# Kernel optimization log

Hardware: AMD Instinct MI355X
Metric: run time of the kernel (lower is better)

Reference implementation:

```python
import jax, jax.numpy as jnp
import numpy as np

IM = 256          # image size (square)
GRID = 512        # oversampled NUFFT grid
J = 6             # Kaiser-Bessel kernel width (torchkbnufft default numpoints)
ALPHA = GRID / IM
BETA = float(np.pi * np.sqrt((J / ALPHA) ** 2 * (ALPHA - 0.5) ** 2 - 0.8))  # Fessler 'best' beta
SC0 = float(np.sinh(BETA) / BETA)
B, C = 1, 8
N_SPOKES, N_SAMPLES = 256, 512
K = N_SPOKES * N_SAMPLES


def _scale_2d():
    # deapodization (inverse FT of KB kernel), separable, normalized to 1 at center
    n = (jnp.arange(IM) - IM / 2) / GRID
    t = BETA ** 2 - (np.pi * J * n) ** 2
    sp = jnp.sqrt(jnp.maximum(t, 1e-12))
    sn = jnp.sqrt(jnp.maximum(-t, 1e-12))
    ft = jnp.where(t > 0, jnp.sinh(sp) / sp, jnp.sinc(sn / np.pi))
    sc = (SC0 / ft).astype(jnp.float32)
    return sc[:, None] * sc[None, :]  # (IM, IM)


def _interp_coords(ktraj):
    # ktraj (2, K) in [-pi, pi] -> J neighbor grid indices + KB weights per dim
    tm = ktraj * (GRID / (2.0 * np.pi))
    base = jnp.floor(tm - J / 2.0)
    j = jnp.arange(1, J + 1, dtype=tm.dtype)
    idx = base[:, :, None] + j                     # (2, K, J)
    u = tm[:, :, None] - idx                       # kernel-centered distance
    q = jnp.maximum(1.0 - (2.0 * u / J) ** 2, 0.0)
    w = jnp.i0(BETA * jnp.sqrt(q)) / J             # (2, K, J) KB weights
    gi = jnp.mod(idx, GRID).astype(jnp.int32)
    return gi[0], gi[1], w[0], w[1]                # iy, ix, wy, wx


def _nufft_fwd(img, coords, sc2):
    # img (B, C, IM, IM) complex -> (B, C, K) non-uniform k-space, 'ortho' norm
    iy, ix, wy, wx = coords
    pad = jnp.zeros(img.shape[:2] + (GRID, GRID), img.dtype)
    pad = pad.at[..., :IM, :IM].set(img * sc2)
    kg = jnp.fft.fft2(pad) / GRID                  # /sqrt(GRID*GRID)
    vals = kg[..., iy[:, :, None], ix[:, None, :]]           # (B,C,K,J,J)
    w2 = (wy[:, :, None] * wx[:, None, :]).astype(kg.dtype)  # (K,J,J)
    return jnp.sum(vals * w2, axis=(-2, -1))


def _nufft_adj(kdata, coords, sc2, smaps):
    # kdata (B, C, K) -> coil-combined image (B, 1, IM, IM), 'ortho' norm
    iy, ix, wy, wx = coords
    w2 = (wy[:, :, None] * wx[:, None, :]).astype(kdata.dtype)
    vals = (kdata[..., None, None] * w2).reshape(kdata.shape[:2] + (-1,))
    flat = (iy[:, :, None] * GRID + ix[:, None, :]).reshape(-1)
    grid = jnp.zeros(kdata.shape[:2] + (GRID * GRID,), kdata.dtype)
    grid = grid.at[:, :, flat].add(vals).reshape(kdata.shape[:2] + (GRID, GRID))
    img = jnp.fft.ifft2(grid) * GRID               # adjoint of fft2/GRID
    img = img[..., :IM, :IM] * sc2
    return jnp.sum(jnp.conj(smaps) * img, axis=1, keepdims=True)


def setup_inputs() -> dict:
    key = jax.random.key(0)
    ks = jax.random.split(key, 6)
    # golden-angle radial trajectory (2, K) in [-pi, pi]
    ga = np.pi * (3.0 - np.sqrt(5.0))
    ang = np.arange(N_SPOKES) * ga
    r = np.linspace(-np.pi, np.pi, N_SAMPLES, endpoint=False)
    ky = np.outer(np.sin(ang), r).reshape(-1)
    kx = np.outer(np.cos(ang), r).reshape(-1)
    ktraj = jnp.asarray(np.stack([ky, kx]), dtype=jnp.float32)
    return {
        "x": jax.random.normal(ks[0], (B, 1, IM, IM), jnp.float32),
        "y_real": jax.random.normal(ks[1], (B, C, K), jnp.float32),
        "y_imag": jax.random.normal(ks[2], (B, C, K), jnp.float32),
        "smaps_real": jax.random.normal(ks[3], (B, C, IM, IM), jnp.float32),
        "smaps_imag": jax.random.normal(ks[4], (B, C, IM, IM), jnp.float32),
        "ktraj": ktraj,
        "lambda_raw": jnp.full((1,), float(np.log(np.exp(1.0) - 1.0)), jnp.float32),
    }


def reference(x, y_real, y_imag, smaps_real, smaps_imag, ktraj, lambda_raw):
    sc2 = _scale_2d()
    coords = _interp_coords(ktraj)
    smaps = (smaps_real + 1j * smaps_imag).astype(jnp.complex64)
    y = (y_real + 1j * y_imag).astype(jnp.complex64)
    x_c = x.astype(jnp.complex64)
    coil_images = x_c * smaps                      # (B, C, IM, IM)
    A_x = _nufft_fwd(coil_images, coords, sc2)     # (B, C, K)
    lam = jax.nn.sigmoid(lambda_raw)[0].astype(jnp.complex64)
    k_dc = lam * A_x + (1.0 - lam) * y             # data consistency mix
    return _nufft_adj(k_dc, coords, sc2, smaps)    # (B, 1, IM, IM) complex64
```

## Files before the change

### kernel.cpp

```cpp
#include <hip/hip_runtime.h>
#include <math.h>

#define GRID_N 512
#define IM_N   256
#define NCOIL  8
#define NK     131072
#define PLANE  (GRID_N*GRID_N)
#define JW     6
#define NBIN   (GRID_N*GRID_N/512*512)
#define WSZ    11
#define NWIN   47
#define ACCROWS 528
#define BETA_F 13.8551003f
#define KSCALE 81.48733086305042f

struct cplx { float x, y; };

__device__ __forceinline__ float bessel_i0f(float x){
  if (x < 3.75f){
    float t = x*(1.0f/3.75f); t = t*t;
    return 1.0f + t*(3.5156229f + t*(3.0899424f + t*(1.2067492f
           + t*(0.2659732f + t*(0.0360768f + t*0.0045813f)))));
  } else {
    float t = 3.75f/x;
    float p = 0.39894228f + t*(0.01328592f + t*(0.00225319f + t*(-0.00157565f
            + t*(0.00916281f + t*(-0.02057706f + t*(0.02635537f
            + t*(-0.01647633f + t*0.00392377f)))))));
    return p * __expf(x) * rsqrtf(x);
  }
}

__device__ __forceinline__ float kb_w(float u){
  float uu = u*(1.0f/3.0f);
  float q = fmaxf(1.0f - uu*uu, 0.0f);
  return bessel_i0f(BETA_F*sqrtf(q)) * (1.0f/6.0f);
}

__device__ __forceinline__ unsigned bf16_of(float f){
  unsigned u = __float_as_uint(f);
  return (u + 0x8000u) >> 16;
}
__device__ __forceinline__ float bf_lo(unsigned w){ return __uint_as_float(w << 16); }
__device__ __forceinline__ float bf_hi(unsigned w){ return __uint_as_float(w & 0xFFFF0000u); }

__global__ void k_sc_table(float* sc){
  int i = threadIdx.x;
  if (i >= IM_N) return;
  float n  = (i - IM_N*0.5f) * (1.0f/GRID_N);
  float pj = 3.14159265358979f * (float)JW * n;
  float t  = BETA_F*BETA_F - pj*pj;
  float sp = sqrtf(fmaxf(t, 1e-12f));
  float sn = sqrtf(fmaxf(-t, 1e-12f));
  float ft = (t > 0.0f) ? (sinhf(sp)/sp) : (sinf(sn)/sn);
  float sc0 = sinhf(BETA_F)/BETA_F;
  sc[i] = sc0/ft;
}

__global__ void k_zero1(float* p, int n){
  int i = blockIdx.x*blockDim.x + threadIdx.x;
  if (i < n) p[i] = 0.f;
}

__global__ void k_fft_fill(const float* __restrict__ ximg, const float* __restrict__ sr,
                           const float* __restrict__ si, const float* __restrict__ sc,
                           cplx* __restrict__ buf){
  __shared__ cplx lds[GRID_N];
  int blk = blockIdx.x;
  int c = blk >> 9, y = blk & (GRID_N-1);
  cplx* p = buf + (size_t)blk * GRID_N;
  int tid = threadIdx.x;
  if (y >= IM_N){
    cplx z; z.x = 0.f; z.y = 0.f;
    for (int i = tid; i < GRID_N; i += 256) p[i] = z;
    return;
  }
  float scy = sc[y];
  for (int i = tid; i < GRID_N; i += 256){
    int r = __brev((unsigned)i) >> 23;
    cplx v; v.x = 0.f; v.y = 0.f;
    if (i < IM_N){
      float vv = ximg[(y<<8)|i] * scy * sc[i];
      int gi = (c << 16) | (y << 8) | i;
      v.x = vv * sr[gi]; v.y = vv * si[gi];
    }
    lds[r] = v;
  }
  __syncthreads();
  for (int half = 1; half < GRID_N; half <<= 1){
    int j = tid & (half-1);
    int k = ((tid & ~(half-1)) << 1) | j;
    float ang = -3.14159265358979f * (float)j / (float)half;
    float sw, cw; __sincosf(ang, &sw, &cw);
    cplx u = lds[k];
    cplx v = lds[k+half];
    cplx t; t.x = v.x*cw - v.y*sw; t.y = v.x*sw + v.y*cw;
    lds[k].x      = u.x + t.x; lds[k].y      = u.y + t.y;
    lds[k+half].x = u.x - t.x; lds[k+half].y = u.y - t.y;
    __syncthreads();
  }
  for (int i = tid; i < GRID_N; i += 256) p[i] = lds[i];
}

template<int DIR>
__global__ void k_fft_rows(cplx* __restrict__ buf, float scale){
  __shared__ cplx lds[GRID_N];
  cplx* p = buf + (size_t)blockIdx.x * GRID_N;
  int tid = threadIdx.x;
  for (int i = tid; i < GRID_N; i += 256){
    int r = __brev((unsigned)i) >> 23;
    lds[r] = p[i];
  }
  __syncthreads();
  for (int half = 1; half < GRID_N; half <<= 1){
    int j = tid & (half-1);
    int k = ((tid & ~(half-1)) << 1) | j;
    float ang = (float)DIR * 3.14159265358979f * (float)j / (float)half;
    float sw, cw; __sincosf(ang, &sw, &cw);
    cplx u = lds[k];
    cplx v = lds[k+half];
    cplx t; t.x = v.x*cw - v.y*sw; t.y = v.x*sw + v.y*cw;
    lds[k].x      = u.x + t.x; lds[k].y      = u.y + t.y;
    lds[k+half].x = u.x - t.x; lds[k+half].y = u.y - t.y;
    __syncthreads();
  }
  for (int i = tid; i < GRID_N; i += 256){
    cplx v = lds[i]; v.x *= scale; v.y *= scale; p[i] = v;
  }
}

__global__ void k_transpose(const cplx* __restrict__ in, cplx* __restrict__ out){
  __shared__ cplx tile[32][33];
  int c  = blockIdx.z;
  int x0 = blockIdx.x*32, y0 = blockIdx.y*32;
  const cplx* ip = in  + (size_t)c*PLANE;
  cplx*       op = out + (size_t)c*PLANE;
  int tx = threadIdx.x, ty = threadIdx.y;
  for (int dy = 0; dy < 32; dy += 8)
    tile[ty+dy][tx] = ip[(size_t)(y0+ty+dy)*GRID_N + (x0+tx)];
  __syncthreads();
  for (int dy = 0; dy < 32; dy += 8)
    op[(size_t)(x0+ty+dy)*GRID_N + (y0+tx)] = tile[tx][ty+dy];
}

__global__ void k_c2i(const float2* __restrict__ plan, float2* __restrict__ inter){
  int t = blockIdx.x*blockDim.x + threadIdx.x;
  if (t >= PLANE*NCOIL) return;
  int c = t & 7; int cell = t >> 3;
  inter[(size_t)cell*8 + c] = plan[(size_t)c*PLANE + cell];
}

__global__ __launch_bounds__(256) void k_fwd(
    const float* __restrict__ ktraj, const float* __restrict__ yre,
    const float* __restrict__ yim, const float* __restrict__ lraw,
    const float4* __restrict__ KTi4, float4* __restrict__ kdc4){
  int t = blockIdx.x*blockDim.x + threadIdx.x;
  if (t >= NK*4) return;
  int k = t >> 2, p = t & 3;

  int iy[JW], ix[JW]; float wy[JW], wx[JW];
  {
    float tm = ktraj[k] * KSCALE;
    int base = (int)floorf(tm - 3.0f);
    #pragma unroll
    for (int j = 1; j <= JW; ++j){
      int fidx = base + j;
      wy[j-1] = kb_w(tm - (float)fidx);
      iy[j-1] = fidx & (GRID_N-1);
    }
  }
  {
    float tm = ktraj[NK + k] * KSCALE;
    int base = (int)floorf(tm - 3.0f);
    #pragma unroll
    for (int j = 1; j <= JW; ++j){
      int fidx = base + j;
      wx[j-1] = kb_w(tm - (float)fidx);
      ix[j-1] = fidx & (GRID_N-1);
    }
  }

  float ax=0.f, ay=0.f, az=0.f, aw=0.f;
  #pragma unroll
  for (int jx = 0; jx < JW; ++jx){
    int ox = ix[jx]*GRID_N;
    #pragma unroll
    for (int jy = 0; jy < JW; ++jy){
      float w2 = wx[jx]*wy[jy];
      float4 v = KTi4[(size_t)(ox + iy[jy])*4 + p];
      ax += w2*v.x; ay += w2*v.y; az += w2*v.z; aw += w2*v.w;
    }
  }
  float lam = 1.0f/(1.0f + __expf(-lraw[0]));
  float oml = 1.0f - lam;
  int c0 = 2*p;
  float4 o;
  o.x = lam*ax + oml*yre[(size_t)c0*NK + k];
  o.y = lam*ay + oml*yim[(size_t)c0*NK + k];
  o.z = lam*az + oml*yre[(size_t)(c0+1)*NK + k];
  o.w = lam*aw + oml*yim[(size_t)(c0+1)*NK + k];
  kdc4[(size_t)k*4 + p] = o;
}

__global__ void k_hist2(const float* __restrict__ ktraj, unsigned* __restrict__ hist2){
  int k = blockIdx.x*blockDim.x + threadIdx.x;
  if (k >= NK) return;
  float tmy = ktraj[k] * KSCALE;
  int by = ((int)floorf(tmy - 3.0f)) & (GRID_N-1);
  float tmx = ktraj[NK + k] * KSCALE;
  int bx = (int)floorf(tmx - 3.0f);
  #pragma unroll
  for (int j = 1; j <= JW; ++j){
    int cj = (bx + j) & (GRID_N-1);
    atomicAdd(&hist2[cj*GRID_N + by], 1u);
  }
}

__global__ void k_colscan(const unsigned* __restrict__ hist2,
                          unsigned* __restrict__ binOff,
                          unsigned* __restrict__ colTotal){
  __shared__ unsigned s[GRID_N];
  int col = blockIdx.x, t = threadIdx.x;
  unsigned mine = hist2[col*GRID_N + t];
  s[t] = mine;
  __syncthreads();
  for (int off = 1; off < GRID_N; off <<= 1){
    unsigned add = (t >= off) ? s[t - off] : 0u;
    __syncthreads();
    s[t] += add;
    __syncthreads();
  }
  binOff[col*GRID_N + t] = s[t] - mine;
  if (t == GRID_N-1) colTotal[col] = s[t];
}

__global__ void k_scanCT(const unsigned* __restrict__ colTotal,
                         unsigned* __restrict__ colBase){
  __shared__ unsigned s[GRID_N];
  int t = threadIdx.x;
  unsigned mine = colTotal[t];
  s[t] = mine;
  __syncthreads();
  for (int off = 1; off < GRID_N; off <<= 1){
    unsigned add = (t >= off) ? s[t - off] : 0u;
    __syncthreads();
    s[t] += add;
    __syncthreads();
  }
  colBase[t] = s[t] - mine;
  if (t == GRID_N-1) colBase[GRID_N] = s[t];
}

__global__ void k_addbase(unsigned* __restrict__ binOff,
                          const unsigned* __restrict__ colBase){
  int i = blockIdx.x*blockDim.x + threadIdx.x;
  if (i > NBIN) return;
  if (i == NBIN){ binOff[i] = colBase[GRID_N]; return; }
  binOff[i] += colBase[i >> 9];
}

__global__ void k_place(const float* __restrict__ ktraj,
                        const unsigned* __restrict__ binOff,
                        unsigned* __restrict__ cnt2,
                        uint4* __restrict__ recs){
  int k = blockIdx.x*blockDim.x + threadIdx.x;
  if (k >= NK) return;
  float tmy = ktraj[k] * KSCALE;
  int by0 = (int)floorf(tmy - 3.0f);
  int by = by0 & (GRID_N-1);
  float wy[JW];
  #pragma unroll
  for (int j = 1; j <= JW; ++j) wy[j-1] = kb_w(tmy - (float)(by0 + j));

  float tmx = ktraj[NK + k] * KSCALE;
  int bx = (int)floorf(tmx - 3.0f);
  unsigned tag = ((unsigned)k << 9) | (unsigned)by;
  #pragma unroll
  for (int j = 1; j <= JW; ++j){
    int cj = (bx + j) & (GRID_N-1);
    float wx = kb_w(tmx - (float)(bx + j));
    uint4 rec;
    rec.x = bf16_of(wx*wy[0]) | (bf16_of(wx*wy[1]) << 16);
    rec.y = bf16_of(wx*wy[2]) | (bf16_of(wx*wy[3]) << 16);
    rec.z = bf16_of(wx*wy[4]) | (bf16_of(wx*wy[5]) << 16);
    rec.w = tag;
    int bin = cj*GRID_N + by;
    unsigned pos = binOff[bin] + atomicAdd(&cnt2[bin], 1u);
    recs[pos] = rec;
  }
}

__global__ __launch_bounds__(512) void k_adj(
    const uint4* __restrict__ recs, const unsigned* __restrict__ binOff,
    const float* __restrict__ kdcf, cplx* __restrict__ Hp){
  __shared__ float accs[ACCROWS*8];
  __shared__ float part[2][8][16][8];
  const int col = blockIdx.x, h = blockIdx.y;
  const int tid = threadIdx.x;
  const int wave = tid >> 6, lane = tid & 63;
  const int slot = lane >> 3, q = lane & 7;
  for (int i = tid; i < ACCROWS*8; i += 512) accs[i] = 0.f;
  __syncthreads();

  const unsigned* bo = binOff + (size_t)col*GRID_N;
  const size_t qoff = (size_t)(h*8 + q);
  int pb = 0;

  for (int wi = 0; wi < NWIN; ++wi){
    int b0 = wi*WSZ;
    int b1 = b0 + WSZ; if (b1 > GRID_N) b1 = GRID_N;
    unsigned s = bo[b0];
    unsigned e = bo[b1];
    if (s == e) continue;

    float a0=0.f,a1=0.f,a2=0.f,a3=0.f,a4=0.f,a5=0.f,a6=0.f,a7=0.f;
    float a8=0.f,a9=0.f,a10=0.f,a11=0.f,a12=0.f,a13=0.f,a14=0.f,a15=0.f;

    for (unsigned base = s + (unsigned)wave*8; base < e; base += 64){
      unsigned e0 = base + (unsigned)slot;
      uint4 rc = recs[e0];
      float vv = 0.f;
      if (e0 < e){
        unsigned kk = (rc.w >> 9) & (NK-1);
        vv = kdcf[(size_t)kk*16 + qoff];
      }
      float w1 = bf_lo(rc.x), w2 = bf_hi(rc.x);
      float w3 = bf_lo(rc.y), w4 = bf_hi(rc.y);
      float w5 = bf_lo(rc.z), w6 = bf_hi(rc.z);
      int off = (int)(rc.w & (GRID_N-1)) - b0;
      #pragma unroll
      for (int r = 0; r < 16; ++r){
        int idx = r - off;
        float wlo = (idx < 2) ? w1 : ((idx < 4) ? w3 : w5);
        float whi = (idx < 2) ? w2 : ((idx < 4) ? w4 : w6);
        float w = (idx & 1) ? whi : wlo;
        w = ((unsigned)idx < 6u) ? w : 0.f;
        float contrib = w * vv;
        if (r==0) a0+=contrib; else if (r==1) a1+=contrib;
        else if (r==2) a2+=contrib; else if (r==3) a3+=contrib;
        else if (r==4) a4+=contrib; else if (r==5) a5+=contrib;
        else if (r==6) a6+=contrib; else if (r==7) a7+=contrib;
        else if (r==8) a8+=contrib; else if (r==9) a9+=contrib;
        else if (r==10) a10+=contrib; else if (r==11) a11+=contrib;
        else if (r==12) a12+=contrib; else if (r==13) a13+=contrib;
        else if (r==14) a14+=contrib; else a15+=contrib;
      }
    }

    #pragma unroll
    for (int m = 8; m <= 32; m <<= 1){
      a0 += __shfl_xor(a0, m);  a1 += __shfl_xor(a1, m);
      a2 += __shfl_xor(a2, m);  a3 += __shfl_xor(a3, m);
      a4 += __shfl_xor(a4, m);  a5 += __shfl_xor(a5, m);
      a6 += __shfl_xor(a6, m);  a7 += __shfl_xor(a7, m);
      a8 += __shfl_xor(a8, m);  a9 += __shfl_xor(a9, m);
      a10 += __shfl_xor(a10, m); a11 += __shfl_xor(a11, m);
      a12 += __shfl_xor(a12, m); a13 += __shfl_xor(a13, m);
      a14 += __shfl_xor(a14, m); a15 += __shfl_xor(a15, m);
    }
    if (slot == 0){
      part[pb][wave][0][q]  = a0;  part[pb][wave][1][q]  = a1;
      part[pb][wave][2][q]  = a2;  part[pb][wave][3][q]  = a3;
      part[pb][wave][4][q]  = a4;  part[pb][wave][5][q]  = a5;
      part[pb][wave][6][q]  = a6;  part[pb][wave][7][q]  = a7;
      part[pb][wave][8][q]  = a8;  part[pb][wave][9][q]  = a9;
      part[pb][wave][10][q] = a10; part[pb][wave][11][q] = a11;
      part[pb][wave][12][q] = a12; part[pb][wave][13][q] = a13;
      part[pb][wave][14][q] = a14; part[pb][wave][15][q] = a15;
    }
    __syncthreads();
    if (tid < 128){
      int r = tid >> 3, qq = tid & 7;
      float sum = part[pb][0][r][qq] + part[pb][1][r][qq]
                + part[pb][2][r][qq] + part[pb][3][r][qq]
                + part[pb][4][r][qq] + part[pb][5][r][qq]
                + part[pb][6][r][qq] + part[pb][7][r][qq];
      accs[(size_t)(b0+1+r)*8 + qq] += sum;
    }
    pb ^= 1;
  }
  __syncthreads();

  for (int i = tid; i < GRID_N*4; i += 512){
    int j = i >> 9, y = i & (GRID_N-1);
    float re = accs[y*8 + 2*j]     + ((y < 16) ? accs[(GRID_N+y)*8 + 2*j]   : 0.f);
    float im = accs[y*8 + 2*j + 1] + ((y < 16) ? accs[(GRID_N+y)*8 + 2*j+1] : 0.f);
    cplx o; o.x = re; o.y = im;
    Hp[(size_t)(h*4 + j)*PLANE + (size_t)col*GRID_N + y] = o;
  }
}

__global__ void k_final(const cplx* __restrict__ Bg, const float* __restrict__ sr,
                        const float* __restrict__ si, const float* __restrict__ sc,
                        float* __restrict__ out, int pairs){
  int idx = blockIdx.x*blockDim.x + threadIdx.x;
  if (idx >= IM_N*IM_N) return;
  int y = idx >> 8, x = idx & 255;
  float s2 = sc[y]*sc[x];
  float ax = 0.f, ay = 0.f;
  #pragma unroll
  for (int c = 0; c < NCOIL; ++c){
    cplx v = Bg[(size_t)c*PLANE + y*GRID_N + x];
    int gi = (c << 16) | idx;
    float rr = sr[gi], ii = si[gi];
    ax += rr*v.x + ii*v.y;
    ay += rr*v.y - ii*v.x;
  }
  if (pairs){
    out[idx*2]   += ax * s2;
    out[idx*2+1] += ay * s2;
  } else {
    out[idx]     += ax * s2;
  }
}

__global__ void k_zero4(float4* p, int n4){
  int i = blockIdx.x*blockDim.x + threadIdx.x;
  if (i < n4) p[i] = make_float4(0.f,0.f,0.f,0.f);
}

__global__ void k_fill_fb(const float* __restrict__ ximg, const float* __restrict__ sr,
                          const float* __restrict__ si, const float* __restrict__ sc,
                          cplx* __restrict__ A){
  int idx = blockIdx.x*blockDim.x + threadIdx.x;
  if (idx >= NCOIL*IM_N*IM_N) return;
  int c = idx >> 16;
  int pix = idx & 65535;
  int y = pix >> 8, x = pix & 255;
  float v = ximg[pix] * sc[y]*sc[x];
  cplx o; o.x = v * sr[idx]; o.y = v * si[idx];
  A[(size_t)c*PLANE + y*GRID_N + x] = o;
}

__global__ void k_gather_scatter_fb(const float* __restrict__ ktraj,
                                    const float* __restrict__ yre,
                                    const float* __restrict__ yim,
                                    const float* __restrict__ lraw,
                                    const cplx* __restrict__ KT,
                                    float* __restrict__ HT){
  int k = blockIdx.x*blockDim.x + threadIdx.x;
  if (k >= NK) return;
  float lam   = 1.0f/(1.0f + __expf(-lraw[0]));
  float omlam = 1.0f - lam;
  int iy[JW], ix[JW]; float wy[JW], wx[JW];
  {
    float tm = ktraj[k] * KSCALE;
    int base = (int)floorf(tm - 3.0f);
    #pragma unroll
    for (int j = 1; j <= JW; ++j){
      wy[j-1] = kb_w(tm - (float)(base+j));
      iy[j-1] = (base+j) & (GRID_N-1);
    }
  }
  {
    float tm = ktraj[NK + k] * KSCALE;
    int base = (int)floorf(tm - 3.0f);
    #pragma unroll
    for (int j = 1; j <= JW; ++j){
      wx[j-1] = kb_w(tm - (float)(base+j));
      ix[j-1] = (base+j) & (GRID_N-1);
    }
  }
  float accx[NCOIL], accy[NCOIL];
  #pragma unroll
  for (int c = 0; c < NCOIL; ++c){ accx[c]=0.f; accy[c]=0.f; }
  #pragma unroll
  for (int jx = 0; jx < JW; ++jx){
    int ox = ix[jx]*GRID_N;
    #pragma unroll
    for (int jy = 0; jy < JW; ++jy){
      float w2 = wx[jx]*wy[jy];
      size_t o = (size_t)(ox + iy[jy]);
      #pragma unroll
      for (int c = 0; c < NCOIL; ++c){
        cplx v = KT[(size_t)c*PLANE + o];
        accx[c] += w2*v.x; accy[c] += w2*v.y;
      }
    }
  }
  float kdx[NCOIL], kdy[NCOIL];
  #pragma unroll
  for (int c = 0; c < NCOIL; ++c){
    kdx[c] = lam*accx[c] + omlam*yre[(size_t)c*NK + k];
    kdy[c] = lam*accy[c] + omlam*yim[(size_t)c*NK + k];
  }
  #pragma unroll
  for (int jx = 0; jx < JW; ++jx){
    int ox = ix[jx]*GRID_N;
    #pragma unroll
    for (int jy = 0; jy < JW; ++jy){
      float w2 = wx[jx]*wy[jy];
      size_t o = (size_t)(ox + iy[jy]);
      #pragma unroll
      for (int c = 0; c < NCOIL; ++c){
        float* dst = HT + ((size_t)c*PLANE + o)*2;
        atomicAdd(dst,   w2*kdx[c]);
        atomicAdd(dst+1, w2*kdy[c]);
      }
    }
  }
}

extern "C" void kernel_launch(void* const* d_in, const int* in_sizes, int n_in,
                              void* d_out, int out_size, void* d_ws, size_t ws_size,
                              hipStream_t stream) {
  const float* ximg  = (const float*)d_in[0];
  const float* yre   = (const float*)d_in[1];
  const float* yim   = (const float*)d_in[2];
  const float* sre   = (const float*)d_in[3];
  const float* sim   = (const float*)d_in[4];
  const float* ktraj = (const float*)d_in[5];
  const float* lraw  = (const float*)d_in[6];
  float* out = (float*)d_out;

  char* ws = (char*)d_ws;
  const size_t REG = 16777216;
  int pairs = (out_size >= 2*IM_N*IM_N) ? 1 : 0;

  const size_t need = 3*REG + 4096;

  if (ws_size >= need){
    cplx*     A     = (cplx*)ws;
    cplx*     Bb    = (cplx*)(ws + REG);
    float4*   KTi4  = (float4*)(ws + 2*REG);
    float*    sc    = (float*)(ws + 3*REG);
    float4*   kdc4  = (float4*)ws;
    unsigned* hist2 = (unsigned*)(ws + 8388608);
    unsigned* binOff= (unsigned*)(ws + 9437184);
    unsigned* cnt2  = (unsigned*)(ws + 10534912);
    unsigned* colTot= (unsigned*)(ws + 11583488);
    unsigned* colBase=(unsigned*)(ws + 11585536);
    uint4*    recs  = (uint4*)(ws + REG);
    cplx*     Hp    = (cplx*)(ws + 2*REG);
    cplx*     imgF  = (cplx*)ws;

    k_sc_table<<<1,256,0,stream>>>(sc);

    k_fft_fill<<<NCOIL*GRID_N,256,0,stream>>>(ximg, sre, sim, sc, A);
    k_transpose<<<dim3(16,16,NCOIL),dim3(32,8),0,stream>>>(A, Bb);
    k_fft_rows<-1><<<NCOIL*GRID_N,256,0,stream>>>(Bb, 1.0f/(float)GRID_N);

    k_c2i<<<(PLANE*NCOIL+255)/256,256,0,stream>>>((const float2*)Bb, (float2*)KTi4);

    k_fwd<<<(NK*4+255)/256,256,0,stream>>>(ktraj, yre, yim, lraw, KTi4, kdc4);

    k_zero1<<<(NBIN+255)/256,256,0,stream>>>((float*)hist2, NBIN);
    k_zero1<<<(NBIN+255)/256,256,0,stream>>>((float*)cnt2,  NBIN);
    k_hist2<<<NK/256,256,0,stream>>>(ktraj, hist2);
    k_colscan<<<GRID_N,GRID_N,0,stream>>>(hist2, binOff, colTot);
    k_scanCT<<<1,GRID_N,0,stream>>>(colTot, colBase);
    k_addbase<<<(NBIN+256)/256,256,0,stream>>>(binOff, colBase);
    k_place<<<NK/256,256,0,stream>>>(ktraj, binOff, cnt2, recs);

    k_adj<<<dim3(GRID_N,2),512,0,stream>>>(recs, binOff, (const float*)kdc4, Hp);

    k_fft_rows<+1><<<NCOIL*GRID_N,256,0,stream>>>(Hp, 1.0f);
    k_transpose<<<dim3(16,16,NCOIL),dim3(32,8),0,stream>>>(Hp, imgF);
    k_fft_rows<+1><<<NCOIL*GRID_N,256,0,stream>>>(imgF, 1.0f/(float)GRID_N);

    k_zero1<<<(out_size+255)/256,256,0,stream>>>(out, out_size);
    k_final<<<(IM_N*IM_N+255)/256,256,0,stream>>>(imgF, sre, sim, sc, out, pairs);
  } else {
    float* sc = (float*)ws;
    cplx*  A  = (cplx*)(ws + 4096);
    cplx*  Bb = (cplx*)(ws + 4096 + REG);
    const int n4 = NCOIL*PLANE*2/4;

    k_sc_table<<<1,256,0,stream>>>(sc);
    k_zero4<<<(n4+255)/256,256,0,stream>>>((float4*)A, n4);
    k_fill_fb<<<(NCOIL*IM_N*IM_N+255)/256,256,0,stream>>>(ximg, sre, sim, sc, A);
    k_fft_rows<-1><<<NCOIL*GRID_N,256,0,stream>>>(A, 1.0f);
    k_transpose<<<dim3(16,16,NCOIL),dim3(32,8),0,stream>>>(A, Bb);
    k_fft_rows<-1><<<NCOIL*GRID_N,256,0,stream>>>(Bb, 1.0f/(float)GRID_N);
    k_zero4<<<(n4+255)/256,256,0,stream>>>((float4*)A, n4);
    k_gather_scatter_fb<<<(NK+255)/256,256,0,stream>>>(ktraj, yre, yim, lraw, Bb, (float*)A);
    k_fft_rows<+1><<<NCOIL*GRID_N,256,0,stream>>>(A, 1.0f);
    k_transpose<<<dim3(16,16,NCOIL),dim3(32,8),0,stream>>>(A, Bb);
    k_fft_rows<+1><<<NCOIL*GRID_N,256,0,stream>>>(Bb, 1.0f/(float)GRID_N);
    k_zero1<<<(out_size+255)/256,256,0,stream>>>(out, out_size);
    k_final<<<(IM_N*IM_N+255)/256,256,0,stream>>>(Bb, sre, sim, sc, out, pairs);
  }
}
```

Before: 395.9 us.

## Merge adjoint coil halves into one block and crop final FFT to image region

The adjoint gridding kernel now handles all 8 coils (16 real channels) per block instead of splitting them across two blocks. Each sample record and its bin offsets are therefore read once rather than twice, at the cost of doubling LDS accumulators and dropping the double-buffered partial array in favor of an extra barrier. The final inverse FFT pass transposes only the half of the grid that maps to the image and runs row FFTs on just the 256 needed rows, writing 256 outputs each. The two histogram zeroing launches are also merged into one by making the buffers contiguous.

```diff
diff --git a/kernel.cpp b/kernel.cpp
--- a/kernel.cpp
+++ b/kernel.cpp
@@ -128,6 +128,34 @@
   }
 }
 
+__global__ void k_fft_rows_c(cplx* __restrict__ buf, float scale){
+  __shared__ cplx lds[GRID_N];
+  int b = blockIdx.x;
+  int c = b >> 8, y = b & (IM_N-1);
+  cplx* p = buf + (size_t)c*PLANE + (size_t)y*GRID_N;
+  int tid = threadIdx.x;
+  for (int i = tid; i < GRID_N; i += 256){
+    int r = __brev((unsigned)i) >> 23;
+    lds[r] = p[i];
+  }
+  __syncthreads();
+  for (int half = 1; half < GRID_N; half <<= 1){
+    int j = tid & (half-1);
+    int k = ((tid & ~(half-1)) << 1) | j;
+    float ang = 3.14159265358979f * (float)j / (float)half;
+    float sw, cw; __sincosf(ang, &sw, &cw);
+    cplx u = lds[k];
+    cplx v = lds[k+half];
+    cplx t; t.x = v.x*cw - v.y*sw; t.y = v.x*sw + v.y*cw;
+    lds[k].x      = u.x + t.x; lds[k].y      = u.y + t.y;
+    lds[k+half].x = u.x - t.x; lds[k+half].y = u.y - t.y;
+    __syncthreads();
+  }
+  for (int i = tid; i < IM_N; i += 256){
+    cplx v = lds[i]; v.x *= scale; v.y *= scale; p[i] = v;
+  }
+}
+
 __global__ void k_transpose(const cplx* __restrict__ in, cplx* __restrict__ out){
   __shared__ cplx tile[32][33];
   int c  = blockIdx.z;
@@ -292,18 +320,16 @@
 __global__ __launch_bounds__(512) void k_adj(
     const uint4* __restrict__ recs, const unsigned* __restrict__ binOff,
     const float* __restrict__ kdcf, cplx* __restrict__ Hp){
-  __shared__ float accs[ACCROWS*8];
-  __shared__ float part[2][8][16][8];
-  const int col = blockIdx.x, h = blockIdx.y;
+  __shared__ float accs[ACCROWS*16];
+  __shared__ float part[8][16][16];
+  const int col = blockIdx.x;
   const int tid = threadIdx.x;
   const int wave = tid >> 6, lane = tid & 63;
-  const int slot = lane >> 3, q = lane & 7;
-  for (int i = tid; i < ACCROWS*8; i += 512) accs[i] = 0.f;
+  const int slot = lane >> 4, q = lane & 15;
+  for (int i = tid; i < ACCROWS*16; i += 512) accs[i] = 0.f;
   __syncthreads();
 
   const unsigned* bo = binOff + (size_t)col*GRID_N;
-  const size_t qoff = (size_t)(h*8 + q);
-  int pb = 0;
 
   for (int wi = 0; wi < NWIN; ++wi){
     int b0 = wi*WSZ;
@@ -315,13 +341,13 @@
     float a0=0.f,a1=0.f,a2=0.f,a3=0.f,a4=0.f,a5=0.f,a6=0.f,a7=0.f;
     float a8=0.f,a9=0.f,a10=0.f,a11=0.f,a12=0.f,a13=0.f,a14=0.f,a15=0.f;
 
-    for (unsigned base = s + (unsigned)wave*8; base < e; base += 64){
+    for (unsigned base = s + (unsigned)wave*4; base < e; base += 32){
       unsigned e0 = base + (unsigned)slot;
       uint4 rc = recs[e0];
       float vv = 0.f;
       if (e0 < e){
         unsigned kk = (rc.w >> 9) & (NK-1);
-        vv = kdcf[(size_t)kk*16 + qoff];
+        vv = kdcf[(size_t)kk*16 + q];
       }
       float w1 = bf_lo(rc.x), w2 = bf_hi(rc.x);
       float w3 = bf_lo(rc.y), w4 = bf_hi(rc.y);
@@ -347,7 +373,7 @@
     }
 
     #pragma unroll
-    for (int m = 8; m <= 32; m <<= 1){
+    for (int m = 16; m <= 32; m <<= 1){
       a0 += __shfl_xor(a0, m);  a1 += __shfl_xor(a1, m);
       a2 += __shfl_xor(a2, m);  a3 += __shfl_xor(a3, m);
       a4 += __shfl_xor(a4, m);  a5 += __shfl_xor(a5, m);
@@ -358,34 +384,32 @@
       a14 += __shfl_xor(a14, m); a15 += __shfl_xor(a15, m);
     }
     if (slot == 0){
-      part[pb][wave][0][q]  = a0;  part[pb][wave][1][q]  = a1;
-      part[pb][wave][2][q]  = a2;  part[pb][wave][3][q]  = a3;
-      part[pb][wave][4][q]  = a4;  part[pb][wave][5][q]  = a5;
-      part[pb][wave][6][q]  = a6;  part[pb][wave][7][q]  = a7;
-      part[pb][wave][8][q]  = a8;  part[pb][wave][9][q]  = a9;
-      part[pb][wave][10][q] = a10; part[pb][wave][11][q] = a11;
-      part[pb][wave][12][q] = a12; part[pb][wave][13][q] = a13;
-      part[pb][wave][14][q] = a14; part[pb][wave][15][q] = a15;
-    }
-    __syncthreads();
-    if (tid < 128){
-      int r = tid >> 3, qq = tid & 7;
-      float sum = part[pb][0][r][qq] + part[pb][1][r][qq]
-                + part[pb][2][r][qq] + part[pb][3][r][qq]
-                + part[pb][4][r][qq] + part[pb][5][r][qq]
-                + part[pb][6][r][qq] + part[pb][7][r][qq];
-      accs[(size_t)(b0+1+r)*8 + qq] += sum;
-    }
-    pb ^= 1;
-  }
-  __syncthreads();
-
-  for (int i = tid; i < GRID_N*4; i += 512){
+      part[wave][0][q]  = a0;  part[wave][1][q]  = a1;
+      part[wave][2][q]  = a2;  part[wave][3][q]  = a3;
+      part[wave][4][q]  = a4;  part[wave][5][q]  = a5;
+      part[wave][6][q]  = a6;  part[wave][7][q]  = a7;
+      part[wave][8][q]  = a8;  part[wave][9][q]  = a9;
+      part[wave][10][q] = a10; part[wave][11][q] = a11;
+      part[wave][12][q] = a12; part[wave][13][q] = a13;
+      part[wave][14][q] = a14; part[wave][15][q] = a15;
+    }
+    __syncthreads();
+    if (tid < 256){
+      int r = tid >> 4, qq = tid & 15;
+      float sum = part[0][r][qq] + part[1][r][qq] + part[2][r][qq]
+                + part[3][r][qq] + part[4][r][qq] + part[5][r][qq]
+                + part[6][r][qq] + part[7][r][qq];
+      accs[(size_t)(b0+1+r)*16 + qq] += sum;
+    }
+    __syncthreads();
+  }
+
+  for (int i = tid; i < GRID_N*8; i += 512){
     int j = i >> 9, y = i & (GRID_N-1);
-    float re = accs[y*8 + 2*j]     + ((y < 16) ? accs[(GRID_N+y)*8 + 2*j]   : 0.f);
-    float im = accs[y*8 + 2*j + 1] + ((y < 16) ? accs[(GRID_N+y)*8 + 2*j+1] : 0.f);
+    float re = accs[y*16 + 2*j]     + ((y < 16) ? accs[(GRID_N+y)*16 + 2*j]   : 0.f);
+    float im = accs[y*16 + 2*j + 1] + ((y < 16) ? accs[(GRID_N+y)*16 + 2*j+1] : 0.f);
     cplx o; o.x = re; o.y = im;
-    Hp[(size_t)(h*4 + j)*PLANE + (size_t)col*GRID_N + y] = o;
+    Hp[(size_t)j*PLANE + (size_t)col*GRID_N + y] = o;
   }
 }
 
@@ -525,10 +549,10 @@
     float*    sc    = (float*)(ws + 3*REG);
     float4*   kdc4  = (float4*)ws;
     unsigned* hist2 = (unsigned*)(ws + 8388608);
-    unsigned* binOff= (unsigned*)(ws + 9437184);
-    unsigned* cnt2  = (unsigned*)(ws + 10534912);
-    unsigned* colTot= (unsigned*)(ws + 11583488);
-    unsigned* colBase=(unsigned*)(ws + 11585536);
+    unsigned* cnt2  = (unsigned*)(ws + 9437184);
+    unsigned* binOff= (unsigned*)(ws + 10485760);
+    unsigned* colTot= (unsigned*)(ws + 11538432);
+    unsigned* colBase=(unsigned*)(ws + 11540480);
     uint4*    recs  = (uint4*)(ws + REG);
     cplx*     Hp    = (cplx*)(ws + 2*REG);
     cplx*     imgF  = (cplx*)ws;
@@ -543,19 +567,18 @@
 
     k_fwd<<<(NK*4+255)/256,256,0,stream>>>(ktraj, yre, yim, lraw, KTi4, kdc4);
 
-    k_zero1<<<(NBIN+255)/256,256,0,stream>>>((float*)hist2, NBIN);
-    k_zero1<<<(NBIN+255)/256,256,0,stream>>>((float*)cnt2,  NBIN);
+    k_zero1<<<(2*NBIN+255)/256,256,0,stream>>>((float*)hist2, 2*NBIN);
     k_hist2<<<NK/256,256,0,stream>>>(ktraj, hist2);
     k_colscan<<<GRID_N,GRID_N,0,stream>>>(hist2, binOff, colTot);
     k_scanCT<<<1,GRID_N,0,stream>>>(colTot, colBase);
     k_addbase<<<(NBIN+256)/256,256,0,stream>>>(binOff, colBase);
     k_place<<<NK/256,256,0,stream>>>(ktraj, binOff, cnt2, recs);
 
-    k_adj<<<dim3(GRID_N,2),512,0,stream>>>(recs, binOff, (const float*)kdc4, Hp);
+    k_adj<<<GRID_N,512,0,stream>>>(recs, binOff, (const float*)kdc4, Hp);
 
     k_fft_rows<+1><<<NCOIL*GRID_N,256,0,stream>>>(Hp, 1.0f);
-    k_transpose<<<dim3(16,16,NCOIL),dim3(32,8),0,stream>>>(Hp, imgF);
-    k_fft_rows<+1><<<NCOIL*GRID_N,256,0,stream>>>(imgF, 1.0f/(float)GRID_N);
+    k_transpose<<<dim3(8,16,NCOIL),dim3(32,8),0,stream>>>(Hp, imgF);
+    k_fft_rows_c<<<NCOIL*IM_N,256,0,stream>>>(imgF, 1.0f/(float)GRID_N);
 
     k_zero1<<<(out_size+255)/256,256,0,stream>>>(out, out_size);
     k_final<<<(IM_N*IM_N+255)/256,256,0,stream>>>(imgF, sre, sim, sc, out, pairs);
```

Measured after the change: 397.9 us. Within noise of the previous version (+0.5%).
